# Optimization experiments

Hardware: AMD Instinct MI355X
Metric: run time of the kernel (lower is better)

Reference implementation:

```python
import jax, jax.numpy as jnp
import numpy as np

N_NODES = 100000
N_EDGES = 600000
IN_DIM = 128
HID = 128
OUT = 256
N_GRAPHS = 256


def setup_inputs() -> dict:
    key = jax.random.key(0)
    ks = jax.random.split(key, 16)
    def w(k, fin, fout):
        return jax.random.normal(k, (fin, fout), dtype=jnp.float32) / np.sqrt(fin).astype(np.float32)
    inp = {
        'x': jax.random.normal(ks[0], (N_NODES, IN_DIM), dtype=jnp.float32),
        'edge_index': jax.random.randint(ks[1], (2, N_EDGES), 0, N_NODES, dtype=jnp.int64) if jax.config.jax_enable_x64 else jax.random.randint(ks[1], (2, N_EDGES), 0, N_NODES, dtype=jnp.int32),
        'graph_batch': jnp.sort(jax.random.randint(ks[2], (N_NODES,), 0, N_GRAPHS, dtype=jnp.int32)),
        # SAGE layer 1 (lin_l: aggregated neighbors, lin_r: root)
        'W1l': w(ks[3], IN_DIM, HID), 'W1r': w(ks[4], IN_DIM, HID), 'b1': jnp.zeros((HID,), jnp.float32),
        'g1': jnp.ones((HID,), jnp.float32), 'be1': jnp.zeros((HID,), jnp.float32),
        # SAGE layer 2
        'W2l': w(ks[5], HID, HID), 'W2r': w(ks[6], HID, HID), 'b2': jnp.zeros((HID,), jnp.float32),
        'g2': jnp.ones((HID,), jnp.float32), 'be2': jnp.zeros((HID,), jnp.float32),
        # SAGE layer 3
        'W3l': w(ks[7], HID, HID), 'W3r': w(ks[8], HID, HID), 'b3': jnp.zeros((HID,), jnp.float32),
        'g3': jnp.ones((HID,), jnp.float32), 'be3': jnp.zeros((HID,), jnp.float32),
        # readout MLP: Linear(2H -> H), ReLU, Linear(H -> OUT)
        'Wr1': w(ks[9], 2 * HID, HID), 'br1': jnp.zeros((HID,), jnp.float32),
        'Wr2': w(ks[10], HID, OUT), 'br2': jnp.zeros((OUT,), jnp.float32),
    }
    return inp


def _layer_norm(h, g, b, eps=1e-5):
    mu = jnp.mean(h, axis=-1, keepdims=True)
    var = jnp.mean(jnp.square(h - mu), axis=-1, keepdims=True)
    return (h - mu) * jax.lax.rsqrt(var + eps) * g + b


def _sage(h, src, dst, Wl, Wr, b):
    # mean-aggregate neighbor features (messages flow src -> dst)
    agg = jax.ops.segment_sum(h[src], dst, num_segments=N_NODES)
    cnt = jax.ops.segment_sum(jnp.ones((src.shape[0],), h.dtype), dst, num_segments=N_NODES)
    mean = agg / jnp.maximum(cnt, 1.0)[:, None]
    return mean @ Wl + h @ Wr + b


def reference(x, edge_index, graph_batch,
              W1l, W1r, b1, g1, be1,
              W2l, W2r, b2, g2, be2,
              W3l, W3r, b3, g3, be3,
              Wr1, br1, Wr2, br2):
    src, dst = edge_index[0], edge_index[1]
    h = jax.nn.relu(_layer_norm(_sage(x, src, dst, W1l, W1r, b1), g1, be1))
    h = jax.nn.relu(_layer_norm(_sage(h, src, dst, W2l, W2r, b2), g2, be2))
    h = jax.nn.relu(_layer_norm(_sage(h, src, dst, W3l, W3r, b3), g3, be3))
    # global mean/max pool per graph
    s = jax.ops.segment_sum(h, graph_batch, num_segments=N_GRAPHS)
    n = jax.ops.segment_sum(jnp.ones((h.shape[0],), h.dtype), graph_batch, num_segments=N_GRAPHS)
    gmean = s / jnp.maximum(n, 1.0)[:, None]
    gmax = jax.ops.segment_max(h, graph_batch, num_segments=N_GRAPHS)
    pooled = jnp.concatenate([gmean, gmax], axis=-1)  # [G, 2H]
    emb = jax.nn.relu(pooled @ Wr1 + br1) @ Wr2 + br2  # [G, OUT]
    norm = jnp.linalg.norm(emb, axis=-1, keepdims=True)
    return emb / jnp.maximum(norm, 1e-12)
```

## Files before the change

### kernel.cpp

```cpp
#include <hip/hip_runtime.h>
#include <hip/hip_bf16.h>

#define N_NODES 100000
#define N_EDGES 600000
#define HID 128
#define OUT_DIM 256
#define N_GRAPHS 256
#define BN 32
#define LDA 260
#define CHUNK 16
#define SCAN_B 512
#define SCAN_NB ((N_NODES + SCAN_B) / SCAN_B)

typedef __attribute__((ext_vector_type(8))) __bf16 bf16x8;
typedef __attribute__((ext_vector_type(4))) float f32x4;

__device__ inline f32x4 mfma16(bf16x8 a, bf16x8 b, f32x4 c) {
    return __builtin_amdgcn_mfma_f32_16x16x32_bf16(a, b, c, 0, 0, 0);
}

__device__ inline unsigned short bf_bits(__bf16 b) {
    union { __bf16 b; unsigned short u; } x; x.b = b; return x.u;
}

__global__ void count_kernel(const int* __restrict__ dst, int* __restrict__ deg) {
    int e = blockIdx.x * blockDim.x + threadIdx.x;
    if (e < N_EDGES) atomicAdd(&deg[dst[e]], 1);
}

__global__ __launch_bounds__(SCAN_B) void scan1_kernel(
    const int* __restrict__ deg, int* __restrict__ part, int* __restrict__ bsum)
{
    __shared__ int s[SCAN_B];
    int t = threadIdx.x;
    int i = blockIdx.x * SCAN_B + t;
    int v = (i < N_NODES) ? deg[i] : 0;
    s[t] = v;
    __syncthreads();
    #pragma unroll
    for (int off = 1; off < SCAN_B; off <<= 1) {
        int x = (t >= off) ? s[t - off] : 0;
        __syncthreads();
        s[t] += x;
        __syncthreads();
    }
    part[i] = s[t] - v;
    if (t == SCAN_B - 1) bsum[blockIdx.x] = s[t];
}

__global__ __launch_bounds__(256) void scan2_kernel(
    const int* __restrict__ bsum, int* __restrict__ boff)
{
    __shared__ int s[256];
    int t = threadIdx.x;
    int v = (t < SCAN_NB) ? bsum[t] : 0;
    s[t] = v;
    __syncthreads();
    #pragma unroll
    for (int off = 1; off < 256; off <<= 1) {
        int x = (t >= off) ? s[t - off] : 0;
        __syncthreads();
        s[t] += x;
        __syncthreads();
    }
    if (t < SCAN_NB) boff[t] = s[t] - v;
}

__global__ __launch_bounds__(SCAN_B) void scan3_kernel(
    const int* __restrict__ part, const int* __restrict__ boff,
    const int* __restrict__ deg,
    int* __restrict__ row_ptr, int* __restrict__ cursor, float* __restrict__ invdeg)
{
    int i = blockIdx.x * SCAN_B + threadIdx.x;
    int rp = part[i] + boff[blockIdx.x];
    if (i <= N_NODES) row_ptr[i] = rp;
    if (i < N_NODES) {
        cursor[i] = rp;
        invdeg[i] = 1.0f / (float)max(deg[i], 1);
    }
}

__global__ void fill_kernel(const int* __restrict__ src, const int* __restrict__ dst,
                            int* __restrict__ cursor, int* __restrict__ csr_src)
{
    int e = blockIdx.x * blockDim.x + threadIdx.x;
    if (e < N_EDGES) {
        int t = dst[e];
        int pos = atomicAdd(&cursor[t], 1);
        csr_src[pos] = src[e];
    }
}

__global__ __launch_bounds__(256) void prep_w(const float* __restrict__ Wl,
                                              const float* __restrict__ Wr,
                                              unsigned short* __restrict__ wf)
{
    int flat = blockIdx.x * 256 + threadIdx.x;
    int j  = flat & 7;
    int l  = (flat >> 3) & 63;
    int nf = (flat >> 9) & 7;
    int ks = flat >> 12;
    int k = ks * 32 + ((l >> 4) << 3) + j;
    int c = nf * 16 + (l & 15);
    float v = (k < HID) ? Wl[k * HID + c] : Wr[(k - HID) * HID + c];
    __bf16 hi = (__bf16)v;
    __bf16 lo = (__bf16)(v - (float)hi);
    wf[flat]         = bf_bits(hi);
    wf[32768 + flat] = bf_bits(lo);
}

__global__ __launch_bounds__(256, 4) void sage_mfma(
    const float* __restrict__ h_in,
    const int* __restrict__ row_ptr, const int* __restrict__ csr_src,
    const float* __restrict__ invdeg,
    const unsigned short* __restrict__ wf,
    const float* __restrict__ bias, const float* __restrict__ gamma,
    const float* __restrict__ beta,
    float* __restrict__ h_out)
{
    __shared__ float smA[BN * LDA];
    __shared__ float lnred[BN][4][2];

    const int tid  = threadIdx.x;
    const int lane = tid & 63;
    const int w    = tid >> 6;
    const int lq   = lane & 15;
    const int lg   = lane >> 4;
    const int node0 = blockIdx.x * BN;

    for (int i = tid; i < BN * 32; i += 256) {
        int n = i >> 5, c = (i & 31) * 4;
        float4 v = *(const float4*)(h_in + (size_t)(node0 + n) * HID + c);
        *(float4*)&smA[n * LDA + HID + c] = v;
    }

    {
        const int half = lane >> 5;
        const int hl   = lane & 31;
        const int d0   = hl * 4;
        for (int n = w * 8; n < w * 8 + 8; ++n) {
            int node = node0 + n;
            f32x4 a0 = {0.f, 0.f, 0.f, 0.f}, a1 = a0, a2 = a0, a3 = a0;
            int e = row_ptr[node], r1 = row_ptr[node + 1];
            for (; e + 8 <= r1; e += 8) {
                int s0 = csr_src[e     + half];
                int s1 = csr_src[e + 2 + half];
                int s2 = csr_src[e + 4 + half];
                int s3 = csr_src[e + 6 + half];
                a0 += *(const f32x4*)(h_in + (size_t)s0 * HID + d0);
                a1 += *(const f32x4*)(h_in + (size_t)s1 * HID + d0);
                a2 += *(const f32x4*)(h_in + (size_t)s2 * HID + d0);
                a3 += *(const f32x4*)(h_in + (size_t)s3 * HID + d0);
            }
            for (; e + 4 <= r1; e += 4) {
                int s0 = csr_src[e     + half];
                int s1 = csr_src[e + 2 + half];
                a0 += *(const f32x4*)(h_in + (size_t)s0 * HID + d0);
                a1 += *(const f32x4*)(h_in + (size_t)s1 * HID + d0);
            }
            for (; e < r1; e += 2) {
                if (e + half < r1) {
                    int s0 = csr_src[e + half];
                    a0 += *(const f32x4*)(h_in + (size_t)s0 * HID + d0);
                }
            }
            f32x4 a = (a0 + a1) + (a2 + a3);
            a.x += __shfl_xor(a.x, 32, 64);
            a.y += __shfl_xor(a.y, 32, 64);
            a.z += __shfl_xor(a.z, 32, 64);
            a.w += __shfl_xor(a.w, 32, 64);
            float inv = invdeg[node];
            a *= inv;
            if (half == 0) *(f32x4*)&smA[n * LDA + d0] = a;
        }
    }
    __syncthreads();

    const int nf0 = w * 2;
    const int col0 = nf0 * 16 + lq;
    const int col1 = col0 + 16;

    f32x4 acc[2][2];
    {
        float b0 = bias[col0], b1 = bias[col1];
        #pragma unroll
        for (int m = 0; m < 2; ++m) {
            acc[m][0] = (f32x4){b0, b0, b0, b0};
            acc[m][1] = (f32x4){b1, b1, b1, b1};
        }
    }

    const bf16x8* wfv = (const bf16x8*)wf;
    #pragma unroll 2
    for (int ks = 0; ks < 8; ++ks) {
        int base = (ks << 9) + nf0 * 64 + lane;
        bf16x8 bh0 = wfv[base];
        bf16x8 bh1 = wfv[base + 64];
        bf16x8 bl0 = wfv[base + 4096];
        bf16x8 bl1 = wfv[base + 4096 + 64];
        #pragma unroll
        for (int m = 0; m < 2; ++m) {
            const float* ap = &smA[(m * 16 + lq) * LDA + (ks << 5) + (lg << 3)];
            float4 a0 = *(const float4*)ap;
            float4 a1 = *(const float4*)(ap + 4);
            float av[8] = {a0.x, a0.y, a0.z, a0.w, a1.x, a1.y, a1.z, a1.w};
            bf16x8 ahi, alo;
            #pragma unroll
            for (int j = 0; j < 8; ++j) {
                __bf16 h = (__bf16)av[j];
                ahi[j] = h;
                alo[j] = (__bf16)(av[j] - (float)h);
            }
            acc[m][0] = mfma16(ahi, bh0, acc[m][0]);
            acc[m][0] = mfma16(alo, bh0, acc[m][0]);
            acc[m][0] = mfma16(ahi, bl0, acc[m][0]);
            acc[m][1] = mfma16(ahi, bh1, acc[m][1]);
            acc[m][1] = mfma16(alo, bh1, acc[m][1]);
            acc[m][1] = mfma16(ahi, bl1, acc[m][1]);
        }
    }

    #pragma unroll
    for (int m = 0; m < 2; ++m) {
        #pragma unroll
        for (int r = 0; r < 4; ++r) {
            float pv = acc[m][0][r] + acc[m][1][r];
            float qv = acc[m][0][r] * acc[m][0][r] + acc[m][1][r] * acc[m][1][r];
            #pragma unroll
            for (int off = 8; off >= 1; off >>= 1) {
                pv += __shfl_xor(pv, off, 64);
                qv += __shfl_xor(qv, off, 64);
            }
            if (lq == 0) {
                int n = m * 16 + lg * 4 + r;
                lnred[n][w][0] = pv;
                lnred[n][w][1] = qv;
            }
        }
    }
    __syncthreads();

    float g0 = gamma[col0], g1 = gamma[col1];
    float be0 = beta[col0], be1 = beta[col1];
    #pragma unroll
    for (int m = 0; m < 2; ++m) {
        #pragma unroll
        for (int r = 0; r < 4; ++r) {
            int n = m * 16 + lg * 4 + r;
            float p = lnred[n][0][0] + lnred[n][1][0] + lnred[n][2][0] + lnred[n][3][0];
            float q = lnred[n][0][1] + lnred[n][1][1] + lnred[n][2][1] + lnred[n][3][1];
            float mu  = p * (1.0f / HID);
            float var = q * (1.0f / HID) - mu * mu;
            float rs = rsqrtf(var + 1e-5f);
            int node = node0 + n;
            float o0 = fmaxf((acc[m][0][r] - mu) * rs * g0 + be0, 0.f);
            float o1 = fmaxf((acc[m][1][r] - mu) * rs * g1 + be1, 0.f);
            h_out[(size_t)node * HID + col0] = o0;
            h_out[(size_t)node * HID + col1] = o1;
        }
    }
}

__global__ __launch_bounds__(128) void pool_kernel(
    const float* __restrict__ h, const int* __restrict__ gb,
    float* __restrict__ gsum, float* __restrict__ gmax, float* __restrict__ gcnt)
{
    int tid = threadIdx.x;
    int start = blockIdx.x * CHUNK;
    if (start >= N_NODES) return;
    int end = min(start + CHUNK, N_NODES);

    int curg = gb[start];
    float s = 0.f, m = 0.f;
    int c = 0;
    for (int node = start; node < end; ++node) {
        int g = gb[node];
        if (g != curg) {
            atomicAdd(&gsum[curg * HID + tid], s);
            atomicMax((int*)&gmax[curg * HID + tid], __float_as_int(m));
            if (tid == 0) atomicAdd(&gcnt[curg], (float)c);
            curg = g; s = 0.f; m = 0.f; c = 0;
        }
        float v = h[(size_t)node * HID + tid];
        s += v;
        m = fmaxf(m, v);
        ++c;
    }
    atomicAdd(&gsum[curg * HID + tid], s);
    atomicMax((int*)&gmax[curg * HID + tid], __float_as_int(m));
    if (tid == 0) atomicAdd(&gcnt[curg], (float)c);
}

__global__ __launch_bounds__(256) void readout_kernel(
    const float* __restrict__ gsum, const float* __restrict__ gmax,
    const float* __restrict__ gcnt,
    const float* __restrict__ Wr1, const float* __restrict__ br1,
    const float* __restrict__ Wr2, const float* __restrict__ br2,
    float* __restrict__ out)
{
    __shared__ float pooled[2 * HID];
    __shared__ float hid[HID];
    __shared__ float red[4];

    int g = blockIdx.x, tid = threadIdx.x;

    if (tid < HID) {
        float n = fmaxf(gcnt[g], 1.0f);
        pooled[tid] = gsum[g * HID + tid] / n;
    } else {
        pooled[tid] = gmax[g * HID + (tid - HID)];
    }
    __syncthreads();

    if (tid < HID) {
        float a = br1[tid];
        for (int k = 0; k < 2 * HID; ++k)
            a += pooled[k] * Wr1[k * HID + tid];
        hid[tid] = fmaxf(a, 0.0f);
    }
    __syncthreads();

    float a = br2[tid];
    for (int k = 0; k < HID; ++k)
        a += hid[k] * Wr2[k * OUT_DIM + tid];

    float ss = a * a;
    #pragma unroll
    for (int off = 32; off >= 1; off >>= 1) ss += __shfl_xor(ss, off, 64);
    int wv = tid >> 6, lane = tid & 63;
    if (lane == 0) red[wv] = ss;
    __syncthreads();
    float tot = red[0] + red[1] + red[2] + red[3];
    float nrm = fmaxf(sqrtf(tot), 1e-12f);
    out[g * OUT_DIM + tid] = a / nrm;
}

extern "C" void kernel_launch(void* const* d_in, const int* in_sizes, int n_in,
                              void* d_out, int out_size, void* d_ws, size_t ws_size,
                              hipStream_t stream) {
    const float* x   = (const float*)d_in[0];
    const int*   ei  = (const int*)d_in[1];
    const int*   gb  = (const int*)d_in[2];
    const float* W1l = (const float*)d_in[3];
    const float* W1r = (const float*)d_in[4];
    const float* b1  = (const float*)d_in[5];
    const float* g1  = (const float*)d_in[6];
    const float* be1 = (const float*)d_in[7];
    const float* W2l = (const float*)d_in[8];
    const float* W2r = (const float*)d_in[9];
    const float* b2  = (const float*)d_in[10];
    const float* g2  = (const float*)d_in[11];
    const float* be2 = (const float*)d_in[12];
    const float* W3l = (const float*)d_in[13];
    const float* W3r = (const float*)d_in[14];
    const float* b3  = (const float*)d_in[15];
    const float* g3  = (const float*)d_in[16];
    const float* be3 = (const float*)d_in[17];
    const float* Wr1 = (const float*)d_in[18];
    const float* br1 = (const float*)d_in[19];
    const float* Wr2 = (const float*)d_in[20];
    const float* br2 = (const float*)d_in[21];

    const int* src = ei;
    const int* dst = ei + N_EDGES;

    char* ws = (char*)d_ws;
    size_t off = 0;
    auto alloc = [&](size_t bytes) -> void* {
        void* p = ws + off;
        off += (bytes + 255) & ~(size_t)255;
        return p;
    };
    float* hA      = (float*)alloc((size_t)N_NODES * HID * 4);
    float* hB      = (float*)alloc((size_t)N_NODES * HID * 4);
    int*   deg     = (int*)alloc((size_t)N_NODES * 4);
    int*   part    = (int*)alloc((size_t)SCAN_NB * SCAN_B * 4);
    int*   bsum    = (int*)alloc((size_t)SCAN_NB * 4);
    int*   boff    = (int*)alloc((size_t)SCAN_NB * 4);
    int*   row_ptr = (int*)alloc((size_t)(N_NODES + 1) * 4);
    int*   cursor  = (int*)alloc((size_t)N_NODES * 4);
    float* invdeg  = (float*)alloc((size_t)N_NODES * 4);
    int*   csr_src = (int*)alloc((size_t)N_EDGES * 4);
    float* gsum    = (float*)alloc((size_t)N_GRAPHS * HID * 4);
    float* gmax    = (float*)alloc((size_t)N_GRAPHS * HID * 4);
    float* gcnt    = (float*)alloc((size_t)N_GRAPHS * 4);
    unsigned short* wf1 = (unsigned short*)alloc(65536 * 2);
    unsigned short* wf2 = (unsigned short*)alloc(65536 * 2);
    unsigned short* wf3 = (unsigned short*)alloc(65536 * 2);

    hipMemsetAsync(deg, 0, (size_t)N_NODES * 4, stream);
    count_kernel<<<(N_EDGES + 255) / 256, 256, 0, stream>>>(dst, deg);
    scan1_kernel<<<SCAN_NB, SCAN_B, 0, stream>>>(deg, part, bsum);
    scan2_kernel<<<1, 256, 0, stream>>>(bsum, boff);
    scan3_kernel<<<SCAN_NB, SCAN_B, 0, stream>>>(part, boff, deg, row_ptr, cursor, invdeg);
    fill_kernel<<<(N_EDGES + 255) / 256, 256, 0, stream>>>(src, dst, cursor, csr_src);

    prep_w<<<128, 256, 0, stream>>>(W1l, W1r, wf1);
    prep_w<<<128, 256, 0, stream>>>(W2l, W2r, wf2);
    prep_w<<<128, 256, 0, stream>>>(W3l, W3r, wf3);

    const int sage_blocks = N_NODES / BN;

    sage_mfma<<<sage_blocks, 256, 0, stream>>>(x,  row_ptr, csr_src, invdeg, wf1, b1, g1, be1, hA);
    sage_mfma<<<sage_blocks, 256, 0, stream>>>(hA, row_ptr, csr_src, invdeg, wf2, b2, g2, be2, hB);
    sage_mfma<<<sage_blocks, 256, 0, stream>>>(hB, row_ptr, csr_src, invdeg, wf3, b3, g3, be3, hA);

    hipMemsetAsync(gsum, 0, (size_t)N_GRAPHS * HID * 4, stream);
    hipMemsetAsync(gmax, 0, (size_t)N_GRAPHS * HID * 4, stream);
    hipMemsetAsync(gcnt, 0, (size_t)N_GRAPHS * 4, stream);
    pool_kernel<<<(N_NODES + CHUNK - 1) / CHUNK, 128, 0, stream>>>(hA, gb, gsum, gmax, gcnt);

    readout_kernel<<<N_GRAPHS, 256, 0, stream>>>(gsum, gmax, gcnt, Wr1, br1, Wr2, br2, (float*)d_out);
}
```

Baseline: 429.4 us.

## Halve SAGE LDS tile, read root features from global, shuffle-broadcast neighbor indices

Stops staging the root-node features in shared memory: the tile now holds only the aggregated mean, and the second half of K in the MFMA loop reads h_in directly from global. This halves LDS use per block and raises the launch bound to 8 blocks per CU to increase occupancy. Neighbor indices for up to 32 edges are loaded once per half-wavefront and broadcast with shuffles instead of repeated csr_src loads, with a fallback loop for higher degrees. The trade-off is extra global traffic in the GEMM phase and possible register pressure under the tighter launch bound.

```diff
diff --git a/kernel.cpp b/kernel.cpp
--- a/kernel.cpp
+++ b/kernel.cpp
@@ -7,7 +7,7 @@
 #define OUT_DIM 256
 #define N_GRAPHS 256
 #define BN 32
-#define LDA 260
+#define LDA2 132
 #define CHUNK 16
 #define SCAN_B 512
 #define SCAN_NB ((N_NODES + SCAN_B) / SCAN_B)
@@ -109,7 +109,7 @@
     wf[32768 + flat] = bf_bits(lo);
 }
 
-__global__ __launch_bounds__(256, 4) void sage_mfma(
+__global__ __launch_bounds__(256, 8) void sage_mfma(
     const float* __restrict__ h_in,
     const int* __restrict__ row_ptr, const int* __restrict__ csr_src,
     const float* __restrict__ invdeg,
@@ -118,7 +118,7 @@
     const float* __restrict__ beta,
     float* __restrict__ h_out)
 {
-    __shared__ float smA[BN * LDA];
+    __shared__ float smA[BN * LDA2];
     __shared__ float lnred[BN][4][2];
 
     const int tid  = threadIdx.x;
@@ -128,50 +128,43 @@
     const int lg   = lane >> 4;
     const int node0 = blockIdx.x * BN;
 
-    for (int i = tid; i < BN * 32; i += 256) {
-        int n = i >> 5, c = (i & 31) * 4;
-        float4 v = *(const float4*)(h_in + (size_t)(node0 + n) * HID + c);
-        *(float4*)&smA[n * LDA + HID + c] = v;
-    }
-
     {
         const int half = lane >> 5;
         const int hl   = lane & 31;
         const int d0   = hl * 4;
         for (int n = w * 8; n < w * 8 + 8; ++n) {
             int node = node0 + n;
+            int r0  = row_ptr[node];
+            int deg = row_ptr[node + 1] - r0;
+            int idx = csr_src[min(r0 + hl, N_EDGES - 1)];
+            int dc  = min(deg, 32);
             f32x4 a0 = {0.f, 0.f, 0.f, 0.f}, a1 = a0, a2 = a0, a3 = a0;
-            int e = row_ptr[node], r1 = row_ptr[node + 1];
-            for (; e + 8 <= r1; e += 8) {
-                int s0 = csr_src[e     + half];
-                int s1 = csr_src[e + 2 + half];
-                int s2 = csr_src[e + 4 + half];
-                int s3 = csr_src[e + 6 + half];
-                a0 += *(const f32x4*)(h_in + (size_t)s0 * HID + d0);
-                a1 += *(const f32x4*)(h_in + (size_t)s1 * HID + d0);
-                a2 += *(const f32x4*)(h_in + (size_t)s2 * HID + d0);
-                a3 += *(const f32x4*)(h_in + (size_t)s3 * HID + d0);
-            }
-            for (; e + 4 <= r1; e += 4) {
-                int s0 = csr_src[e     + half];
-                int s1 = csr_src[e + 2 + half];
-                a0 += *(const f32x4*)(h_in + (size_t)s0 * HID + d0);
-                a1 += *(const f32x4*)(h_in + (size_t)s1 * HID + d0);
-            }
-            for (; e < r1; e += 2) {
-                if (e + half < r1) {
-                    int s0 = csr_src[e + half];
-                    a0 += *(const f32x4*)(h_in + (size_t)s0 * HID + d0);
-                }
+            int s = half;
+            for (; s + 6 < dc; s += 8) {
+                int i0 = __shfl(idx, s,     32);
+                int i1 = __shfl(idx, s + 2, 32);
+                int i2 = __shfl(idx, s + 4, 32);
+                int i3 = __shfl(idx, s + 6, 32);
+                a0 += *(const f32x4*)(h_in + (size_t)i0 * HID + d0);
+                a1 += *(const f32x4*)(h_in + (size_t)i1 * HID + d0);
+                a2 += *(const f32x4*)(h_in + (size_t)i2 * HID + d0);
+                a3 += *(const f32x4*)(h_in + (size_t)i3 * HID + d0);
+            }
+            for (; s < dc; s += 2) {
+                int i0 = __shfl(idx, s, 32);
+                a0 += *(const f32x4*)(h_in + (size_t)i0 * HID + d0);
+            }
+            for (int t2 = 32 + half; t2 < deg; t2 += 2) {
+                int i0 = csr_src[r0 + t2];
+                a0 += *(const f32x4*)(h_in + (size_t)i0 * HID + d0);
             }
             f32x4 a = (a0 + a1) + (a2 + a3);
             a.x += __shfl_xor(a.x, 32, 64);
             a.y += __shfl_xor(a.y, 32, 64);
             a.z += __shfl_xor(a.z, 32, 64);
             a.w += __shfl_xor(a.w, 32, 64);
-            float inv = invdeg[node];
-            a *= inv;
-            if (half == 0) *(f32x4*)&smA[n * LDA + d0] = a;
+            a *= invdeg[node];
+            if (half == 0) *(f32x4*)&smA[n * LDA2 + d0] = a;
         }
     }
     __syncthreads();
@@ -200,9 +193,17 @@
         bf16x8 bl1 = wfv[base + 4096 + 64];
         #pragma unroll
         for (int m = 0; m < 2; ++m) {
-            const float* ap = &smA[(m * 16 + lq) * LDA + (ks << 5) + (lg << 3)];
-            float4 a0 = *(const float4*)ap;
-            float4 a1 = *(const float4*)(ap + 4);
+            float4 a0, a1;
+            if (ks < 4) {
+                const float* ap = &smA[(m * 16 + lq) * LDA2 + (ks << 5) + (lg << 3)];
+                a0 = *(const float4*)ap;
+                a1 = *(const float4*)(ap + 4);
+            } else {
+                const float* rp = h_in + (size_t)(node0 + m * 16 + lq) * HID
+                                + ((ks - 4) << 5) + (lg << 3);
+                a0 = *(const float4*)rp;
+                a1 = *(const float4*)(rp + 4);
+            }
             float av[8] = {a0.x, a0.y, a0.z, a0.w, a1.x, a1.y, a1.z, a1.w};
             bf16x8 ahi, alo;
             #pragma unroll
```

Result: faster. 402.6 us (-6.3%).
